# Performance work log

Measured on AMD Instinct MI355X. Metric: run time of the kernel, lower is better.

The kernel has to match this reference:

```python
import jax, jax.numpy as jnp
import numpy as np

B, N, C = 4096, 49, 128
NUM_HEADS = 4
SCALE = C ** (-0.5)  # NOTE: source uses dim**-0.5, not head_dim**-0.5


def setup_inputs() -> dict:
    key = jax.random.key(0)
    k1, k2, k3 = jax.random.split(key, 3)
    x = jax.random.normal(k1, (B, N, C), dtype=jnp.float32)
    Wqkv = jax.random.normal(k2, (C, 3 * C), dtype=jnp.float32) * 0.02
    bqkv = jnp.zeros((3 * C,), dtype=jnp.float32)
    Wproj = jax.random.normal(k3, (C, C), dtype=jnp.float32) * 0.02
    bproj = jnp.zeros((C,), dtype=jnp.float32)
    return {"x": x, "Wqkv": Wqkv, "bqkv": bqkv, "Wproj": Wproj, "bproj": bproj}


def reference(x, Wqkv, bqkv, Wproj, bproj):
    b, n, c = x.shape
    h = NUM_HEADS
    d = c // h
    qkv = x @ Wqkv + bqkv                      # [B, N, 3C]
    qkv = qkv.reshape(b, n, 3, h, d).transpose(2, 0, 3, 1, 4)  # [3, B, H, N, d]
    q, k, v = qkv[0], qkv[1], qkv[2]
    attn = jnp.einsum("bhnd,bhmd->bhnm", q, k) * SCALE
    attn = jax.nn.softmax(attn, axis=-1)
    out = jnp.einsum("bhnm,bhmd->bhnd", attn, v)  # [B, H, N, d]
    out = out.transpose(0, 2, 1, 3).reshape(b, n, c)
    return out @ Wproj + bproj
```

## Files before the change

kernel.cpp:

```cpp
#include <hip/hip_runtime.h>


#define N_TOK 49
#define R1B 16384
#define SCF (0.08838834764831845f * 1.4426950408889634f)

typedef __attribute__((ext_vector_type(8))) __bf16 bf16x8;
typedef __attribute__((ext_vector_type(4))) __bf16 bf16x4;
typedef __attribute__((ext_vector_type(4))) float  f32x4;
typedef unsigned int uint2v __attribute__((ext_vector_type(2)));

__global__ void pack_weights(const float* __restrict__ Wqkv,
                             const float* __restrict__ Wproj,
                             __bf16* __restrict__ ws) {
    int idx  = blockIdx.x * 256 + threadIdx.x;
    int j    = idx & 7;
    int lane = (idx >> 3) & 63;
    int l16  = lane & 15, g = lane >> 4;
    if (idx < 49152) {
        int frag = idx >> 9;
        int mt = frag >> 2, ks = frag & 3;
        int m = mt * 16 + l16;
        int k = ks * 32 + g * 8 + j;
        float v = Wqkv[k * 384 + m];
        if (m < 128) v *= SCF;
        ws[idx] = (__bf16)v;
    } else {
        int i2 = idx - 49152;
        int frag = i2 >> 9;
        int nt = frag >> 2, ks = frag & 3;
        int n = nt * 16 + l16;
        int k = ks * 32 + g * 8 + j;
        ws[idx] = (__bf16)Wproj[k * 128 + n];
    }
}

__device__ __forceinline__ int x_off(int tok, int ch) {
    return tok * 256 + ((((ch >> 3) ^ (tok & 15))) << 4) + ((ch & 7) << 1);
}
__device__ __forceinline__ int vt_off(int h, int ch, int tok) {
    return h * 4096 + ch * 128 + ((((tok >> 3) ^ (ch & 7))) << 4) + ((tok & 7) << 1);
}
__device__ __forceinline__ int o_off(int tok, int ch) {
    return (ch >> 5) * 4096 + tok * 64 + (((((ch & 31) >> 3) ^ (tok & 3))) << 4) + ((ch & 7) << 1);
}
__device__ __forceinline__ int k_off(int h, int tok, int ch) {
    return R1B + h * 4096 + tok * 64 + ((((ch >> 3) ^ (tok & 3))) << 4) + ((ch & 7) << 1);
}

__device__ __forceinline__ unsigned pk2(float a, float b) {
    union { __bf16 h[2]; unsigned u; } U;
    U.h[0] = (__bf16)a; U.h[1] = (__bf16)b;
    return U.u;
}

__device__ __forceinline__ bf16x8 reorg_pl(unsigned W0, unsigned W1,
                                           unsigned W2, unsigned W3) {
    uint2v a  = __builtin_amdgcn_permlane32_swap(W0, W2, false, false);
    uint2v a2 = __builtin_amdgcn_permlane16_swap(a[0], a[1], false, false);
    uint2v b  = __builtin_amdgcn_permlane32_swap(W1, W3, false, false);
    uint2v b2 = __builtin_amdgcn_permlane16_swap(b[0], b[1], false, false);
    union { unsigned u[4]; bf16x8 v; } U;
    U.u[0] = a2[0]; U.u[1] = b2[0]; U.u[2] = a2[1]; U.u[3] = b2[1];
    return U.v;
}

__global__ __launch_bounds__(256, 4)
void fused_win_attn(const float* __restrict__ x,
                    const float* __restrict__ bqkv,
                    const float* __restrict__ bproj,
                    const __bf16* __restrict__ wpack,
                    float* __restrict__ out) {
    __shared__ __align__(16) char smem[32768];

    const int tid  = threadIdx.x;
    const int w    = tid >> 6;
    const int lane = tid & 63;
    const int l16  = lane & 15;
    const int g    = lane >> 4;
    const int b    = blockIdx.x;
    const float* xb = x + (size_t)b * (N_TOK * 128);

    #pragma unroll
    for (int it = 0; it < 4; ++it) {
        int unit = tid + it * 256;
        int tok = unit >> 4, ch = (unit & 15) * 8;
        f32x4 lo = {0.f, 0.f, 0.f, 0.f}, hi = {0.f, 0.f, 0.f, 0.f};
        if (tok < N_TOK) {
            const float* p = xb + tok * 128 + ch;
            lo = *(const f32x4*)p;
            hi = *(const f32x4*)(p + 4);
        }
        bf16x8 f;
        f[0]=(__bf16)lo[0]; f[1]=(__bf16)lo[1]; f[2]=(__bf16)lo[2]; f[3]=(__bf16)lo[3];
        f[4]=(__bf16)hi[0]; f[5]=(__bf16)hi[1]; f[6]=(__bf16)hi[2]; f[7]=(__bf16)hi[3];
        *(bf16x8*)(smem + x_off(tok, ch)) = f;
    }
    __syncthreads();

    f32x4 bq0 = *(const f32x4*)(bqkv + 32 * w + 0 + 4 * g);   bq0 *= SCF;
    f32x4 bq1 = *(const f32x4*)(bqkv + 32 * w + 16 + 4 * g);  bq1 *= SCF;
    f32x4 bk0 = *(const f32x4*)(bqkv + 128 + 32 * w + 0 + 4 * g);
    f32x4 bk1 = *(const f32x4*)(bqkv + 128 + 32 * w + 16 + 4 * g);
    f32x4 accA[4][4];
    #pragma unroll
    for (int nt = 0; nt < 4; ++nt) {
        accA[0][nt] = bq0; accA[1][nt] = bq1;
        accA[2][nt] = bk0; accA[3][nt] = bk1;
    }
    #pragma unroll
    for (int ks = 0; ks < 4; ++ks) {
        bf16x8 xfr[4];
        #pragma unroll
        for (int nt = 0; nt < 4; ++nt)
            xfr[nt] = *(const bf16x8*)(smem + x_off(16 * nt + l16, 32 * ks + 8 * g));
        #pragma unroll
        for (int m = 0; m < 4; ++m) {
            int mtg = (m < 2) ? (2 * w + m) : (8 + 2 * w + m - 2);
            bf16x8 af = *(const bf16x8*)(wpack + ((mtg * 4 + ks) * 64 + lane) * 8);
            #pragma unroll
            for (int nt = 0; nt < 4; ++nt)
                accA[m][nt] = __builtin_amdgcn_mfma_f32_16x16x32_bf16(af, xfr[nt], accA[m][nt], 0, 0, 0);
        }
    }
    #pragma unroll
    for (int m = 2; m < 4; ++m) {
        const int lch = 16 * (m - 2) + 4 * g;
        #pragma unroll
        for (int nt = 0; nt < 4; ++nt) {
            bf16x4 pk = {(__bf16)accA[m][nt][0], (__bf16)accA[m][nt][1],
                         (__bf16)accA[m][nt][2], (__bf16)accA[m][nt][3]};
            *(bf16x4*)(smem + k_off(w, 16 * nt + l16, lch)) = pk;
        }
    }
    bf16x8 qf[4];
    #pragma unroll
    for (int t = 0; t < 4; ++t)
        qf[t] = reorg_pl(pk2(accA[0][t][0], accA[0][t][1]),
                         pk2(accA[0][t][2], accA[0][t][3]),
                         pk2(accA[1][t][0], accA[1][t][1]),
                         pk2(accA[1][t][2], accA[1][t][3]));

    f32x4 bv0 = *(const f32x4*)(bqkv + 256 + 32 * w + 0 + 4 * g);
    f32x4 bv1 = *(const f32x4*)(bqkv + 256 + 32 * w + 16 + 4 * g);
    f32x4 accB[2][4];
    #pragma unroll
    for (int nt = 0; nt < 4; ++nt) { accB[0][nt] = bv0; accB[1][nt] = bv1; }
    #pragma unroll
    for (int ks = 0; ks < 4; ++ks) {
        bf16x8 xfr[4];
        #pragma unroll
        for (int nt = 0; nt < 4; ++nt)
            xfr[nt] = *(const bf16x8*)(smem + x_off(16 * nt + l16, 32 * ks + 8 * g));
        #pragma unroll
        for (int m = 0; m < 2; ++m) {
            bf16x8 af = *(const bf16x8*)(wpack + (((16 + 2 * w + m) * 4 + ks) * 64 + lane) * 8);
            #pragma unroll
            for (int nt = 0; nt < 4; ++nt)
                accB[m][nt] = __builtin_amdgcn_mfma_f32_16x16x32_bf16(af, xfr[nt], accB[m][nt], 0, 0, 0);
        }
    }
    __syncthreads();

    #pragma unroll
    for (int m = 0; m < 2; ++m) {
        const int vch = 16 * m + 4 * g;
        #pragma unroll
        for (int nt = 0; nt < 4; ++nt) {
            const int T = 16 * nt + l16;
            *(__bf16*)(smem + vt_off(w, vch + 0, T)) = (__bf16)accB[m][nt][0];
            *(__bf16*)(smem + vt_off(w, vch + 1, T)) = (__bf16)accB[m][nt][1];
            *(__bf16*)(smem + vt_off(w, vch + 2, T)) = (__bf16)accB[m][nt][2];
            *(__bf16*)(smem + vt_off(w, vch + 3, T)) = (__bf16)accB[m][nt][3];
        }
    }

    f32x4 s[4][4];
    #pragma unroll
    for (int mt = 0; mt < 4; ++mt) {
        bf16x8 kf = *(const bf16x8*)(smem + k_off(w, 16 * mt + l16, 8 * g));
        #pragma unroll
        for (int nt = 0; nt < 4; ++nt)
            s[mt][nt] = __builtin_amdgcn_mfma_f32_16x16x32_bf16(
                kf, qf[nt], (f32x4){0.f, 0.f, 0.f, 0.f}, 0, 0, 0);
    }

    float r[4];
    #pragma unroll
    for (int nt = 0; nt < 4; ++nt) {
        float sum = 0.f;
        #pragma unroll
        for (int mt = 0; mt < 4; ++mt)
            #pragma unroll
            for (int i = 0; i < 4; ++i) {
                int key = 16 * mt + 4 * g + i;
                float p = (key < N_TOK) ? __builtin_amdgcn_exp2f(s[mt][nt][i]) : 0.f;
                s[mt][nt][i] = p;
                sum += p;
            }
        sum += __shfl_xor(sum, 16);
        sum += __shfl_xor(sum, 32);
        r[nt] = __builtin_amdgcn_rcpf(sum);
    }

    bf16x8 pf[4][2];
    #pragma unroll
    for (int nt = 0; nt < 4; ++nt)
        #pragma unroll
        for (int ks = 0; ks < 2; ++ks)
            pf[nt][ks] = reorg_pl(pk2(s[2 * ks][nt][0], s[2 * ks][nt][1]),
                                  pk2(s[2 * ks][nt][2], s[2 * ks][nt][3]),
                                  pk2(s[2 * ks + 1][nt][0], s[2 * ks + 1][nt][1]),
                                  pk2(s[2 * ks + 1][nt][2], s[2 * ks + 1][nt][3]));

    f32x4 o[2][4];
    #pragma unroll
    for (int m = 0; m < 2; ++m)
        #pragma unroll
        for (int nt = 0; nt < 4; ++nt) o[m][nt] = (f32x4){0.f, 0.f, 0.f, 0.f};
    #pragma unroll
    for (int ks = 0; ks < 2; ++ks)
        #pragma unroll
        for (int m = 0; m < 2; ++m) {
            bf16x8 vf = *(const bf16x8*)(smem + vt_off(w, 16 * m + l16, 32 * ks + 8 * g));
            #pragma unroll
            for (int nt = 0; nt < 4; ++nt)
                o[m][nt] = __builtin_amdgcn_mfma_f32_16x16x32_bf16(
                    vf, pf[nt][ks], o[m][nt], 0, 0, 0);
        }

    #pragma unroll
    for (int m = 0; m < 2; ++m)
        #pragma unroll
        for (int nt = 0; nt < 4; ++nt) {
            bf16x4 pk = {(__bf16)(o[m][nt][0] * r[nt]), (__bf16)(o[m][nt][1] * r[nt]),
                         (__bf16)(o[m][nt][2] * r[nt]), (__bf16)(o[m][nt][3] * r[nt])};
            *(bf16x4*)(smem + o_off(16 * nt + l16, 32 * w + 16 * m + 4 * g)) = pk;
        }

    const __bf16* bp = wpack + 49152;
    bf16x8 bpf[2][4];
    #pragma unroll
    for (int ntp = 0; ntp < 2; ++ntp)
        #pragma unroll
        for (int ks = 0; ks < 4; ++ks)
            bpf[ntp][ks] = *(const bf16x8*)(bp + (((2 * w + ntp) * 4 + ks) * 64 + lane) * 8);
    __syncthreads();

    const float bj0 = bproj[16 * (2 * w + 0) + l16];
    const float bj1 = bproj[16 * (2 * w + 1) + l16];
    f32x4 po[4][2];
    #pragma unroll
    for (int mt = 0; mt < 4; ++mt) {
        po[mt][0] = (f32x4){bj0, bj0, bj0, bj0};
        po[mt][1] = (f32x4){bj1, bj1, bj1, bj1};
    }
    #pragma unroll
    for (int ks = 0; ks < 4; ++ks) {
        #pragma unroll
        for (int mt = 0; mt < 4; ++mt) {
            bf16x8 a = *(const bf16x8*)(smem + o_off(16 * mt + l16, 32 * ks + 8 * g));
            po[mt][0] = __builtin_amdgcn_mfma_f32_16x16x32_bf16(a, bpf[0][ks], po[mt][0], 0, 0, 0);
            po[mt][1] = __builtin_amdgcn_mfma_f32_16x16x32_bf16(a, bpf[1][ks], po[mt][1], 0, 0, 0);
        }
    }
    #pragma unroll
    for (int ntp = 0; ntp < 2; ++ntp) {
        const int och = 16 * (2 * w + ntp) + l16;
        #pragma unroll
        for (int mt = 0; mt < 4; ++mt)
            #pragma unroll
            for (int i = 0; i < 4; ++i) {
                int tok = 16 * mt + 4 * g + i;
                if (tok < N_TOK)
                    out[((size_t)b * N_TOK + tok) * 128 + och] = po[mt][ntp][i];
            }
    }
}

extern "C" void kernel_launch(void* const* d_in, const int* in_sizes, int n_in,
                              void* d_out, int out_size, void* d_ws, size_t ws_size,
                              hipStream_t stream) {
    const float* x     = (const float*)d_in[0];
    const float* Wqkv  = (const float*)d_in[1];
    const float* bqkv  = (const float*)d_in[2];
    const float* Wproj = (const float*)d_in[3];
    const float* bproj = (const float*)d_in[4];
    __bf16* ws  = (__bf16*)d_ws;
    float* outp = (float*)d_out;

    pack_weights<<<256, 256, 0, stream>>>(Wqkv, Wproj, ws);
    fused_win_attn<<<4096, 256, 0, stream>>>(x, bqkv, bproj, ws, outp);
}
```

Before: 85.44 us.

## Replace permlane fragment reshuffles with LDS round-trips and split projection by token rows

Q and softmax probability fragments were rearranged into MFMA B-operand layout with permlane32/16 swaps. They are now written to a per-head shared-memory scratch region and read back in the needed layout. The output projection is also repartitioned so each wave handles one 16-token row tile across all 8 output column tiles, instead of all tokens for two column tiles. This trades register shuffle instructions for extra LDS traffic, and makes each wave load the full projection weight from global/L2.

```diff
diff --git a/kernel.cpp b/kernel.cpp
--- a/kernel.cpp
+++ b/kernel.cpp
@@ -8,7 +8,6 @@
 typedef __attribute__((ext_vector_type(8))) __bf16 bf16x8;
 typedef __attribute__((ext_vector_type(4))) __bf16 bf16x4;
 typedef __attribute__((ext_vector_type(4))) float  f32x4;
-typedef unsigned int uint2v __attribute__((ext_vector_type(2)));
 
 __global__ void pack_weights(const float* __restrict__ Wqkv,
                              const float* __restrict__ Wproj,
@@ -44,25 +43,8 @@
 __device__ __forceinline__ int o_off(int tok, int ch) {
     return (ch >> 5) * 4096 + tok * 64 + (((((ch & 31) >> 3) ^ (tok & 3))) << 4) + ((ch & 7) << 1);
 }
-__device__ __forceinline__ int k_off(int h, int tok, int ch) {
-    return R1B + h * 4096 + tok * 64 + ((((ch >> 3) ^ (tok & 3))) << 4) + ((ch & 7) << 1);
-}
-
-__device__ __forceinline__ unsigned pk2(float a, float b) {
-    union { __bf16 h[2]; unsigned u; } U;
-    U.h[0] = (__bf16)a; U.h[1] = (__bf16)b;
-    return U.u;
-}
-
-__device__ __forceinline__ bf16x8 reorg_pl(unsigned W0, unsigned W1,
-                                           unsigned W2, unsigned W3) {
-    uint2v a  = __builtin_amdgcn_permlane32_swap(W0, W2, false, false);
-    uint2v a2 = __builtin_amdgcn_permlane16_swap(a[0], a[1], false, false);
-    uint2v b  = __builtin_amdgcn_permlane32_swap(W1, W3, false, false);
-    uint2v b2 = __builtin_amdgcn_permlane16_swap(b[0], b[1], false, false);
-    union { unsigned u[4]; bf16x8 v; } U;
-    U.u[0] = a2[0]; U.u[1] = b2[0]; U.u[2] = a2[1]; U.u[3] = b2[1];
-    return U.v;
+__device__ __forceinline__ int sc_off(int h, int row, int col) {
+    return R1B + h * 4096 + row * 64 + ((((col >> 3) ^ (row & 3))) << 4) + ((col & 7) << 1);
 }
 
 __global__ __launch_bounds__(256, 4)
@@ -124,22 +106,29 @@
         }
     }
     #pragma unroll
+    for (int m = 0; m < 2; ++m) {
+        const int lch = 16 * m + 4 * g;
+        #pragma unroll
+        for (int nt = 0; nt < 4; ++nt) {
+            bf16x4 pk = {(__bf16)accA[m][nt][0], (__bf16)accA[m][nt][1],
+                         (__bf16)accA[m][nt][2], (__bf16)accA[m][nt][3]};
+            *(bf16x4*)(smem + sc_off(w, 16 * nt + l16, lch)) = pk;
+        }
+    }
+    bf16x8 qf[4];
+    #pragma unroll
+    for (int t = 0; t < 4; ++t)
+        qf[t] = *(const bf16x8*)(smem + sc_off(w, 16 * t + l16, 8 * g));
+    #pragma unroll
     for (int m = 2; m < 4; ++m) {
         const int lch = 16 * (m - 2) + 4 * g;
         #pragma unroll
         for (int nt = 0; nt < 4; ++nt) {
             bf16x4 pk = {(__bf16)accA[m][nt][0], (__bf16)accA[m][nt][1],
                          (__bf16)accA[m][nt][2], (__bf16)accA[m][nt][3]};
-            *(bf16x4*)(smem + k_off(w, 16 * nt + l16, lch)) = pk;
-        }
-    }
-    bf16x8 qf[4];
-    #pragma unroll
-    for (int t = 0; t < 4; ++t)
-        qf[t] = reorg_pl(pk2(accA[0][t][0], accA[0][t][1]),
-                         pk2(accA[0][t][2], accA[0][t][3]),
-                         pk2(accA[1][t][0], accA[1][t][1]),
-                         pk2(accA[1][t][2], accA[1][t][3]));
+            *(bf16x4*)(smem + sc_off(w, 16 * nt + l16, lch)) = pk;
+        }
+    }
 
     f32x4 bv0 = *(const f32x4*)(bqkv + 256 + 32 * w + 0 + 4 * g);
     f32x4 bv1 = *(const f32x4*)(bqkv + 256 + 32 * w + 16 + 4 * g);
@@ -178,7 +167,7 @@
     f32x4 s[4][4];
     #pragma unroll
     for (int mt = 0; mt < 4; ++mt) {
-        bf16x8 kf = *(const bf16x8*)(smem + k_off(w, 16 * mt + l16, 8 * g));
+        bf16x8 kf = *(const bf16x8*)(smem + sc_off(w, 16 * mt + l16, 8 * g));
         #pragma unroll
         for (int nt = 0; nt < 4; ++nt)
             s[mt][nt] = __builtin_amdgcn_mfma_f32_16x16x32_bf16(
@@ -203,15 +192,13 @@
         r[nt] = __builtin_amdgcn_rcpf(sum);
     }
 
-    bf16x8 pf[4][2];
-    #pragma unroll
-    for (int nt = 0; nt < 4; ++nt)
-        #pragma unroll
-        for (int ks = 0; ks < 2; ++ks)
-            pf[nt][ks] = reorg_pl(pk2(s[2 * ks][nt][0], s[2 * ks][nt][1]),
-                                  pk2(s[2 * ks][nt][2], s[2 * ks][nt][3]),
-                                  pk2(s[2 * ks + 1][nt][0], s[2 * ks + 1][nt][1]),
-                                  pk2(s[2 * ks + 1][nt][2], s[2 * ks + 1][nt][3]));
+    bf16x4 pp[4][4];
+    #pragma unroll
+    for (int mt = 0; mt < 4; ++mt)
+        #pragma unroll
+        for (int nt = 0; nt < 4; ++nt)
+            pp[mt][nt] = (bf16x4){(__bf16)s[mt][nt][0], (__bf16)s[mt][nt][1],
+                                  (__bf16)s[mt][nt][2], (__bf16)s[mt][nt][3]};
 
     f32x4 o[2][4];
     #pragma unroll
@@ -219,15 +206,25 @@
         #pragma unroll
         for (int nt = 0; nt < 4; ++nt) o[m][nt] = (f32x4){0.f, 0.f, 0.f, 0.f};
     #pragma unroll
-    for (int ks = 0; ks < 2; ++ks)
+    for (int ks = 0; ks < 2; ++ks) {
+        #pragma unroll
+        for (int mt = 0; mt < 2; ++mt)
+            #pragma unroll
+            for (int nt = 0; nt < 4; ++nt)
+                *(bf16x4*)(smem + sc_off(w, 16 * nt + l16, 16 * mt + 4 * g)) = pp[2 * ks + mt][nt];
+        bf16x8 pf[4];
+        #pragma unroll
+        for (int nt = 0; nt < 4; ++nt)
+            pf[nt] = *(const bf16x8*)(smem + sc_off(w, 16 * nt + l16, 8 * g));
         #pragma unroll
         for (int m = 0; m < 2; ++m) {
             bf16x8 vf = *(const bf16x8*)(smem + vt_off(w, 16 * m + l16, 32 * ks + 8 * g));
             #pragma unroll
             for (int nt = 0; nt < 4; ++nt)
                 o[m][nt] = __builtin_amdgcn_mfma_f32_16x16x32_bf16(
-                    vf, pf[nt][ks], o[m][nt], 0, 0, 0);
-        }
+                    vf, pf[nt], o[m][nt], 0, 0, 0);
+        }
+    }
 
     #pragma unroll
     for (int m = 0; m < 2; ++m)
@@ -237,44 +234,33 @@
                          (__bf16)(o[m][nt][2] * r[nt]), (__bf16)(o[m][nt][3] * r[nt])};
             *(bf16x4*)(smem + o_off(16 * nt + l16, 32 * w + 16 * m + 4 * g)) = pk;
         }
+    __syncthreads();
 
     const __bf16* bp = wpack + 49152;
-    bf16x8 bpf[2][4];
-    #pragma unroll
-    for (int ntp = 0; ntp < 2; ++ntp)
-        #pragma unroll
-        for (int ks = 0; ks < 4; ++ks)
-            bpf[ntp][ks] = *(const bf16x8*)(bp + (((2 * w + ntp) * 4 + ks) * 64 + lane) * 8);
-    __syncthreads();
-
-    const float bj0 = bproj[16 * (2 * w + 0) + l16];
-    const float bj1 = bproj[16 * (2 * w + 1) + l16];
-    f32x4 po[4][2];
-    #pragma unroll
-    for (int mt = 0; mt < 4; ++mt) {
-        po[mt][0] = (f32x4){bj0, bj0, bj0, bj0};
-        po[mt][1] = (f32x4){bj1, bj1, bj1, bj1};
+    f32x4 po[8];
+    #pragma unroll
+    for (int ntp = 0; ntp < 8; ++ntp) {
+        const float bj = bproj[16 * ntp + l16];
+        po[ntp] = (f32x4){bj, bj, bj, bj};
     }
     #pragma unroll
     for (int ks = 0; ks < 4; ++ks) {
-        #pragma unroll
-        for (int mt = 0; mt < 4; ++mt) {
-            bf16x8 a = *(const bf16x8*)(smem + o_off(16 * mt + l16, 32 * ks + 8 * g));
-            po[mt][0] = __builtin_amdgcn_mfma_f32_16x16x32_bf16(a, bpf[0][ks], po[mt][0], 0, 0, 0);
-            po[mt][1] = __builtin_amdgcn_mfma_f32_16x16x32_bf16(a, bpf[1][ks], po[mt][1], 0, 0, 0);
-        }
-    }
-    #pragma unroll
-    for (int ntp = 0; ntp < 2; ++ntp) {
-        const int och = 16 * (2 * w + ntp) + l16;
-        #pragma unroll
-        for (int mt = 0; mt < 4; ++mt)
-            #pragma unroll
-            for (int i = 0; i < 4; ++i) {
-                int tok = 16 * mt + 4 * g + i;
-                if (tok < N_TOK)
-                    out[((size_t)b * N_TOK + tok) * 128 + och] = po[mt][ntp][i];
-            }
+        bf16x8 a = *(const bf16x8*)(smem + o_off(16 * w + l16, 32 * ks + 8 * g));
+        #pragma unroll
+        for (int ntp = 0; ntp < 8; ++ntp) {
+            bf16x8 bf_ = *(const bf16x8*)(bp + ((ntp * 4 + ks) * 64 + lane) * 8);
+            po[ntp] = __builtin_amdgcn_mfma_f32_16x16x32_bf16(a, bf_, po[ntp], 0, 0, 0);
+        }
+    }
+    #pragma unroll
+    for (int ntp = 0; ntp < 8; ++ntp) {
+        const int och = 16 * ntp + l16;
+        #pragma unroll
+        for (int i = 0; i < 4; ++i) {
+            int tok = 16 * w + 4 * g + i;
+            if (tok < N_TOK)
+                out[((size_t)b * N_TOK + tok) * 128 + och] = po[ntp][i];
+        }
     }
 }
 
```

After: 101.2 us. 1.19x slower.
